# Optimization experiments

Measured on AMD Instinct MI355X. Metric: run time of the kernel, lower is better.

Reference implementation:

```python
import jax, jax.numpy as jnp
import numpy as np

N = 100000   # nodes
E = 1600000  # edges per view
F = 256      # feature_dim
G = 512      # num graphs in batch
H, C = 2, 32 # heads, channels per head (GATConv(F, 32, heads=2))
EPS = 1e-5


def setup_inputs() -> dict:
    key = jax.random.key(0)
    ks = jax.random.split(key, 32)
    def w(i, shape, fan_in):
        return jax.random.normal(ks[i], shape, jnp.float32) / np.sqrt(fan_in)
    inp = {
        "x": jax.random.normal(ks[0], (N, F), jnp.float32),
        "edge_index_ast": jax.random.randint(ks[1], (2, E), 0, N),
        "edge_index_cfg": jax.random.randint(ks[2], (2, E), 0, N),
        "edge_index_pdg": jax.random.randint(ks[3], (2, E), 0, N),
        "batch": jnp.sort(jax.random.randint(ks[4], (N,), 0, G)),
        "num_graphs": G,
        # BatchNorm1d(feature_dim) affine params (training-mode batch stats)
        "bn_w": jnp.ones((F,), jnp.float32),
        "bn_b": jnp.zeros((F,), jnp.float32),
    }
    i = 5
    for v in ("ast", "cfg", "pdg"):
        inp[f"{v}_W"] = w(i, (F, H * C), F); i += 1
        inp[f"{v}_att_src"] = w(i, (H, C), C); i += 1
        inp[f"{v}_att_dst"] = w(i, (H, C), C); i += 1
        inp[f"{v}_bias"] = jnp.zeros((H * C,), jnp.float32)
    inp["g1_w"] = w(i, (64, 32), 64); i += 1
    inp["g1_b"] = jnp.zeros((32,), jnp.float32)
    inp["g2_w"] = w(i, (32, 3), 32); i += 1
    inp["g2_b"] = jnp.zeros((3,), jnp.float32)
    inp["c1_w"] = w(i, (64, 128), 64); i += 1
    inp["c1_b"] = jnp.zeros((128,), jnp.float32)
    inp["c2_w"] = w(i, (128, 64), 128); i += 1
    inp["c2_b"] = jnp.zeros((64,), jnp.float32)
    inp["c3_w"] = w(i, (64, 1), 64); i += 1
    inp["c3_b"] = jnp.zeros((1,), jnp.float32)
    return inp


def _gat(x, edge_index, W, att_src, att_dst, bias):
    """PyG GATConv (shared lin, add_self_loops=True, concat heads)."""
    n = x.shape[0]
    loops = jnp.arange(n)
    src = jnp.concatenate([edge_index[0], loops])
    dst = jnp.concatenate([edge_index[1], loops])
    h = (x @ W).reshape(n, H, C)                       # [N,H,C]
    a_src = jnp.sum(h * att_src, axis=-1)              # [N,H]
    a_dst = jnp.sum(h * att_dst, axis=-1)              # [N,H]
    e = jax.nn.leaky_relu(a_src[src] + a_dst[dst], 0.2)  # [Etot,H]
    m = jax.ops.segment_max(e, dst, num_segments=n)
    p = jnp.exp(e - m[dst])
    denom = jax.ops.segment_sum(p, dst, num_segments=n)
    alpha = p / (denom[dst] + 1e-16)                   # [Etot,H]
    out = jax.ops.segment_sum(h[src] * alpha[:, :, None], dst, num_segments=n)
    return out.reshape(n, H * C) + bias


def reference(x, edge_index_ast, edge_index_cfg, edge_index_pdg, batch, num_graphs,
              bn_w, bn_b,
              ast_W, ast_att_src, ast_att_dst, ast_bias,
              cfg_W, cfg_att_src, cfg_att_dst, cfg_bias,
              pdg_W, pdg_att_src, pdg_att_dst, pdg_bias,
              g1_w, g1_b, g2_w, g2_b,
              c1_w, c1_b, c2_w, c2_b, c3_w, c3_b):
    # input BatchNorm1d (training-mode batch statistics, biased variance)
    mu = x.mean(0)
    var = x.var(0)
    xn = (x - mu) / jnp.sqrt(var + EPS) * bn_w + bn_b

    h_ast = jax.ops.segment_max(jax.nn.elu(_gat(xn, edge_index_ast, ast_W, ast_att_src, ast_att_dst, ast_bias)), batch, num_segments=num_graphs)
    h_cfg = jax.ops.segment_max(jax.nn.elu(_gat(xn, edge_index_cfg, cfg_W, cfg_att_src, cfg_att_dst, cfg_bias)), batch, num_segments=num_graphs)
    h_pdg = jax.ops.segment_max(jax.nn.elu(_gat(xn, edge_index_pdg, pdg_W, pdg_att_src, pdg_att_dst, pdg_bias)), batch, num_segments=num_graphs)

    avg_view = (h_ast + h_cfg + h_pdg) / 3.0
    wts = jax.nn.softmax(jax.nn.relu(avg_view @ g1_w + g1_b) @ g2_w + g2_b, axis=-1)
    fused = wts[:, 0:1] * h_ast + wts[:, 1:2] * h_cfg + wts[:, 2:3] * h_pdg

    # classifier (dropout = identity at inference)
    z = jax.nn.relu(fused @ c1_w + c1_b)
    z = jax.nn.relu(z @ c2_w + c2_b)
    logits = (z @ c3_w + c3_b).reshape(-1)             # [G]
    return logits
```

## Files before the change

kernel.cpp:

```cpp
#include <hip/hip_runtime.h>
#include <hip/hip_bf16.h>
#include <hip/hip_fp16.h>

#define N_NODES 100000
#define N_EDGES 1600000
#define ETOT    (N_EDGES + N_NODES)
#define NE3     (3 * ETOT)
#define N3      (3 * N_NODES)
#define NF      256
#define NG      512
#define NHC     64
#define NOUT3   192
#define BN_EPS  1e-5f

#define NBUCK   586
#define NB1     1024
#define EGRAIN  20
#define ECHUNK  (256 * EGRAIN)
#define SCAN_N  (NBUCK * NB1)
#define ATT2_NB (N_NODES * 16 / 256)

typedef _Float16 f16x8 __attribute__((ext_vector_type(8)));
typedef float    f32x4 __attribute__((ext_vector_type(4)));

__device__ __forceinline__ unsigned fenc(float f){
  unsigned b = __float_as_uint(f);
  return (b & 0x80000000u) ? ~b : (b | 0x80000000u);
}
__device__ __forceinline__ float fdec(unsigned u){
  unsigned b = (u & 0x80000000u) ? (u & 0x7FFFFFFFu) : ~u;
  return __uint_as_float(b);
}
__device__ __forceinline__ float lrelu(float x){ return x > 0.f ? x : 0.2f * x; }
__device__ __forceinline__ float eluf(float x){ return x > 0.f ? x : (__expf(x) - 1.f); }

__global__ void k_init_pooled(unsigned* pooled){
  int i = blockIdx.x * 256 + threadIdx.x;
  if (i < 3 * NG * NHC) pooled[i] = 0x007FFFFFu;
}

#define STATS_NB ((N_NODES + 127) / 128)
__global__ __launch_bounds__(256) void k_pre(const float* __restrict__ x,
                                             float* __restrict__ sums, float* __restrict__ sumsq,
                                             const int* __restrict__ eA, const int* __restrict__ eC,
                                             const int* __restrict__ eP,
                                             int* __restrict__ gcounts){
  int t = threadIdx.x;
  if (blockIdx.x < STATS_NB){
    int r0 = blockIdx.x * 128;
    int rmax = N_NODES - r0; if (rmax > 128) rmax = 128;
    float s = 0.f, q = 0.f;
    for (int r = 0; r < rmax; ++r){
      float v = x[(size_t)(r0 + r) * NF + t];
      s += v; q += v * v;
    }
    atomicAdd(&sums[t], s);
    atomicAdd(&sumsq[t], q);
    return;
  }
  __shared__ int hist[NBUCK];
  int bi = blockIdx.x - STATS_NB;
  for (int b = t; b < NBUCK; b += 256) hist[b] = 0;
  __syncthreads();
  int base = bi * ECHUNK + t;
#pragma unroll
  for (int k = 0; k < EGRAIN; ++k){
    int i = base + k * 256;
    if (i < NE3){
      int v = i / ETOT; int j = i - v * ETOT;
      const int* ei = (v == 0) ? eA : (v == 1) ? eC : eP;
      int d = (j < N_EDGES) ? ei[N_EDGES + j] : (j - N_EDGES);
      int vd = v * N_NODES + d;
      atomicAdd(&hist[vd >> 9], 1);
    }
  }
  __syncthreads();
  for (int b = t; b < NBUCK; b += 256) gcounts[b * NB1 + bi] = hist[b];
}

__global__ __launch_bounds__(256) void k_prep2(const float* __restrict__ sums, const float* __restrict__ sumsq,
                                               const float* __restrict__ bn_w, const float* __restrict__ bn_b,
                                               const float* __restrict__ WA, const float* __restrict__ WC,
                                               const float* __restrict__ WP,
                                               __half* __restrict__ WpT, float* __restrict__ bp){
  __shared__ float red[256];
  int o = blockIdx.x;
  int v = o >> 6, oc = o & 63;
  const float* W = (v == 0) ? WA : (v == 1) ? WC : WP;
  int f = threadIdx.x;
  float mu  = sums[f]  * (1.f / N_NODES);
  float var = sumsq[f] * (1.f / N_NODES) - mu * mu;
  float sc  = bn_w[f] * rsqrtf(var + BN_EPS);
  float sh_ = bn_b[f] - mu * sc;
  float w = W[f * 64 + oc];
  WpT[(size_t)o * NF + f] = __float2half(w * sc);
  red[f] = sh_ * w;
  __syncthreads();
  for (int off = 128; off > 0; off >>= 1){
    if (f < off) red[f] += red[f + off];
    __syncthreads();
  }
  if (f == 0) bp[o] = red[0];
}

__global__ __launch_bounds__(256) void k_avec(const float* __restrict__ sums, const float* __restrict__ sumsq,
                                              const float* __restrict__ bn_w, const float* __restrict__ bn_b,
                                              const float* __restrict__ WA, const float* __restrict__ asA, const float* __restrict__ adA,
                                              const float* __restrict__ WC, const float* __restrict__ asC, const float* __restrict__ adC,
                                              const float* __restrict__ WP, const float* __restrict__ asP, const float* __restrict__ adP,
                                              float* __restrict__ wvec, float* __restrict__ cbias){
  __shared__ float red[256];
  int f = threadIdx.x;
  float mu  = sums[f]  * (1.f / N_NODES);
  float var = sumsq[f] * (1.f / N_NODES) - mu * mu;
  float sc  = bn_w[f] * rsqrtf(var + BN_EPS);
  float sh_ = bn_b[f] - mu * sc;
  for (int v = 0; v < 3; ++v){
    const float* W  = (v == 0) ? WA : (v == 1) ? WC : WP;
    const float* As = (v == 0) ? asA : (v == 1) ? asC : asP;
    const float* Ad = (v == 0) ? adA : (v == 1) ? adC : adP;
    for (int h = 0; h < 2; ++h){
      float sa = 0.f, da = 0.f;
      for (int c = 0; c < 32; ++c){
        float w = W[f * 64 + h * 32 + c];
        sa += w * As[h * 32 + c];
        da += w * Ad[h * 32 + c];
      }
      int q = v * 2 + h;
      wvec[q * NF + f]       = sc * sa;
      wvec[(6 + q) * NF + f] = sc * da;
      red[f] = sh_ * sa; __syncthreads();
      for (int off = 128; off > 0; off >>= 1){ if (f < off) red[f] += red[f + off]; __syncthreads(); }
      if (f == 0) cbias[q] = red[0];
      __syncthreads();
      red[f] = sh_ * da; __syncthreads();
      for (int off = 128; off > 0; off >>= 1){ if (f < off) red[f] += red[f + off]; __syncthreads(); }
      if (f == 0) cbias[6 + q] = red[0];
      __syncthreads();
    }
  }
}

__global__ __launch_bounds__(256) void k_att2(const float* __restrict__ x,
                                              const float* __restrict__ wvec, const float* __restrict__ cbias,
                                              float* __restrict__ a_src, float* __restrict__ a_dst,
                                              unsigned* __restrict__ gpart){
  __shared__ float wv[12][256];
  __shared__ float cb[12];
  __shared__ unsigned samax[6];
  int t = threadIdx.x;
#pragma unroll
  for (int q = 0; q < 12; ++q) wv[q][t] = wvec[q * NF + t];
  if (t < 12) cb[t] = cbias[t];
  if (t < 6) samax[t] = 0u;
  __syncthreads();
  int grp = t >> 4, lid = t & 15;
  int n = blockIdx.x * 16 + grp;
  float4 xr[4];
#pragma unroll
  for (int k = 0; k < 4; ++k)
    xr[k] = *(const float4*)(x + (size_t)n * NF + k * 64 + lid * 4);
  float res[12];
#pragma unroll
  for (int q = 0; q < 12; ++q){
    float acc = 0.f;
#pragma unroll
    for (int k = 0; k < 4; ++k){
      float4 wq = *(const float4*)&wv[q][k * 64 + lid * 4];
      acc += xr[k].x * wq.x + xr[k].y * wq.y + xr[k].z * wq.z + xr[k].w * wq.w;
    }
    acc += __shfl_xor(acc, 1, 16);
    acc += __shfl_xor(acc, 2, 16);
    acc += __shfl_xor(acc, 4, 16);
    acc += __shfl_xor(acc, 8, 16);
    res[q] = acc + cb[q];
  }
  if (lid == 0){
#pragma unroll
    for (int v = 0; v < 3; ++v){
      int g = v * N_NODES + n;
      *(float2*)(a_src + (size_t)g * 2) = make_float2(res[v*2+0], res[v*2+1]);
      *(float2*)(a_dst + (size_t)g * 2) = make_float2(res[6+v*2+0], res[6+v*2+1]);
      atomicMax(&samax[v*2+0], fenc(res[v*2+0]));
      atomicMax(&samax[v*2+1], fenc(res[v*2+1]));
    }
  }
  __syncthreads();
  if (t < 6) gpart[blockIdx.x * 6 + t] = samax[t];
}

__global__ __launch_bounds__(256) void k_amax(const unsigned* __restrict__ gpart, unsigned* __restrict__ amax){
  __shared__ unsigned sm[6];
  int t = threadIdx.x;
  if (t < 6) sm[t] = 0u;
  __syncthreads();
  unsigned m[6] = {0u, 0u, 0u, 0u, 0u, 0u};
  for (int bi = t; bi < ATT2_NB; bi += 256){
    const unsigned* p = gpart + (size_t)bi * 6;
#pragma unroll
    for (int k = 0; k < 6; ++k) m[k] = max(m[k], p[k]);
  }
#pragma unroll
  for (int k = 0; k < 6; ++k) atomicMax(&sm[k], m[k]);
  __syncthreads();
  if (t < 6) amax[t] = sm[t];
}

__global__ __launch_bounds__(256) void k_scan1(const int* __restrict__ cnt, int* __restrict__ out,
                                               int* __restrict__ bsum, int n){
  __shared__ int sh[256];
  int t = threadIdx.x; int base = blockIdx.x * 2048 + t * 8;
  int v[8]; int s = 0;
#pragma unroll
  for (int i = 0; i < 8; ++i){ v[i] = (base + i < n) ? cnt[base + i] : 0; s += v[i]; }
  sh[t] = s; __syncthreads();
  for (int off = 1; off < 256; off <<= 1){
    int xv = (t >= off) ? sh[t - off] : 0;
    __syncthreads();
    sh[t] += xv;
    __syncthreads();
  }
  int p = sh[t] - s;
  if (t == 255) bsum[blockIdx.x] = sh[255];
#pragma unroll
  for (int i = 0; i < 8; ++i){ if (base + i < n) out[base + i] = p; p += v[i]; }
}

__global__ __launch_bounds__(512) void k_scan2(int* __restrict__ bsum, int* __restrict__ total_out, int nb){
  __shared__ int sh[512];
  int t = threadIdx.x;
  int o = (t < nb) ? bsum[t] : 0;
  sh[t] = o; __syncthreads();
  for (int off = 1; off < 512; off <<= 1){
    int xv = (t >= off) ? sh[t - off] : 0;
    __syncthreads();
    sh[t] += xv;
    __syncthreads();
  }
  if (t < nb) bsum[t] = sh[t] - o;
  if (t == nb - 1) total_out[0] = sh[t];
}

__global__ __launch_bounds__(256) void k_scan3(int* __restrict__ out, const int* __restrict__ bsum, int n){
  int add = bsum[blockIdx.x];
  int base = blockIdx.x * 2048 + threadIdx.x * 8;
#pragma unroll
  for (int i = 0; i < 8; ++i) if (base + i < n) out[base + i] += add;
}

#define GBM 64
#define GEMM_NB ((N_NODES + GBM - 1) / GBM)
__global__ __launch_bounds__(256) void k_fused(const float* __restrict__ x,
                                               const __half* __restrict__ WpT, const float* __restrict__ bp,
                                               __half* __restrict__ h16,
                                               const int* __restrict__ eA, const int* __restrict__ eC,
                                               const int* __restrict__ eP,
                                               const int* __restrict__ gscan, int* __restrict__ packed){
  union U { _Float16 xs[64 * 256]; int pos[NBUCK]; };
  __shared__ U sm;
  int t = threadIdx.x;
  if (blockIdx.x >= GEMM_NB){
    int bi = blockIdx.x - GEMM_NB;
    for (int b = t; b < NBUCK; b += 256) sm.pos[b] = gscan[b * NB1 + bi];
    __syncthreads();
    int base = bi * ECHUNK + t;
#pragma unroll
    for (int k = 0; k < EGRAIN; ++k){
      int i = base + k * 256;
      if (i < NE3){
        int v = i / ETOT; int j = i - v * ETOT;
        const int* ei = (v == 0) ? eA : (v == 1) ? eC : eP;
        int s, d;
        if (j < N_EDGES){ s = ei[j]; d = ei[N_EDGES + j]; } else { s = j - N_EDGES; d = s; }
        int vd = v * N_NODES + d;
        int p = atomicAdd(&sm.pos[vd >> 9], 1);
        packed[p] = s | ((vd & 511) << 17);
      }
    }
    return;
  }
  int m0 = blockIdx.x * GBM;
#pragma unroll
  for (int k = 0; k < 8; ++k){
    int G = t + k * 256;
    int row = G >> 5, g = G & 31;
    int grow = m0 + row; if (grow >= N_NODES) grow = N_NODES - 1;
    const float4* src = (const float4*)(x + (size_t)grow * NF + ((g ^ (row & 7)) << 3));
    float4 lo = src[0], hi = src[1];
    f16x8 h;
    h[0]=(_Float16)lo.x; h[1]=(_Float16)lo.y; h[2]=(_Float16)lo.z; h[3]=(_Float16)lo.w;
    h[4]=(_Float16)hi.x; h[5]=(_Float16)hi.y; h[6]=(_Float16)hi.z; h[7]=(_Float16)hi.w;
    *(f16x8*)&sm.xs[(size_t)G << 3] = h;
  }
  __syncthreads();
  int lane = t & 63, w = t >> 6;
  int lr = lane & 15, lk = lane >> 4;
  int colb = w * 48;
  f32x4 acc[4][3];
#pragma unroll
  for (int mt = 0; mt < 4; ++mt)
#pragma unroll
    for (int ct = 0; ct < 3; ++ct) acc[mt][ct] = (f32x4){0.f, 0.f, 0.f, 0.f};
  float bpv[3];
#pragma unroll
  for (int ct = 0; ct < 3; ++ct) bpv[ct] = bp[colb + ct * 16 + lr];
#pragma unroll
  for (int kk = 0; kk < 8; ++kk){
    int khalf = kk * 32 + lk * 8;
    f16x8 av[4];
#pragma unroll
    for (int mt = 0; mt < 4; ++mt){
      int row = mt * 16 + lr;
      av[mt] = *(const f16x8*)&sm.xs[row * 256 + (khalf ^ ((row & 7) << 3))];
    }
    f16x8 bv[3];
#pragma unroll
    for (int ct = 0; ct < 3; ++ct){
      int col = colb + ct * 16 + lr;
      bv[ct] = *(const f16x8*)(const void*)(WpT + (size_t)col * NF + khalf);
    }
#pragma unroll
    for (int mt = 0; mt < 4; ++mt)
#pragma unroll
      for (int ct = 0; ct < 3; ++ct)
        acc[mt][ct] = __builtin_amdgcn_mfma_f32_16x16x32_f16(av[mt], bv[ct], acc[mt][ct], 0, 0, 0);
  }
#pragma unroll
  for (int mt = 0; mt < 4; ++mt){
#pragma unroll
    for (int r = 0; r < 4; ++r){
      int row = m0 + mt * 16 + lk * 4 + r;
      if (row < N_NODES){
#pragma unroll
        for (int ct = 0; ct < 3; ++ct)
          h16[(size_t)row * NOUT3 + colb + ct * 16 + lr] = __float2half(acc[mt][ct][r] + bpv[ct]);
      }
    }
  }
}

__global__ __launch_bounds__(512) void k_build(const int* __restrict__ gscan, const int* __restrict__ packed,
                                               int* __restrict__ entries, int* __restrict__ offsets){
  __shared__ int hist2[512];
  __shared__ int sh[512];
  int b = blockIdx.x, t = threadIdx.x;
  int base = gscan[b * NB1];
  int end  = (b == NBUCK - 1) ? NE3 : gscan[(b + 1) * NB1];
  hist2[t] = 0;
  __syncthreads();
  for (int i = base + t; i < end; i += 512)
    atomicAdd(&hist2[(packed[i] >> 17) & 511], 1);
  __syncthreads();
  int cnt = hist2[t];
  sh[t] = cnt; __syncthreads();
  for (int off = 1; off < 512; off <<= 1){
    int xv = (t >= off) ? sh[t - off] : 0;
    __syncthreads();
    sh[t] += xv;
    __syncthreads();
  }
  int excl = sh[t] - cnt;
  hist2[t] = excl;
  int vd0 = (b << 9) + t;
  if (vd0 < N3) offsets[vd0] = base + excl;
  if (b == NBUCK - 1 && t == 0) offsets[N3] = NE3;
  __syncthreads();
  for (int i = base + t; i < end; i += 512){
    int pk = packed[i];
    int low = (pk >> 17) & 511;
    int pos = atomicAdd(&hist2[low], 1);
    entries[base + pos] = pk & 0x1FFFF;
  }
}

__global__ __launch_bounds__(256) void k_gather(const int* __restrict__ entries, const int* __restrict__ offsets,
                                                const float* __restrict__ a_src, const float* __restrict__ a_dst,
                                                const unsigned* __restrict__ amax,
                                                const __half* __restrict__ h16,
                                                const float* __restrict__ bA, const float* __restrict__ bC,
                                                const float* __restrict__ bP,
                                                const int* __restrict__ batch, unsigned* __restrict__ pooled){
  __shared__ unsigned red[64];
  __shared__ int kmin, kmax;
  int t = threadIdx.x;
  if (t == 0){ kmin = 0x7FFFFFFF; kmax = -1; }
  if (t < 64) red[t] = 0u;
  __syncthreads();
  int grp = t >> 4;
  int lid = t & 15;
  int g = blockIdx.x * 16 + grp;
  int v = g / N_NODES; int n = g - v * N_NODES;
  int vN = v * N_NODES;
  float ad0 = a_dst[g*2+0], ad1 = a_dst[g*2+1];
  float m0 = lrelu(fdec(amax[v*2+0]) + ad0);
  float m1 = lrelu(fdec(amax[v*2+1]) + ad1);
  int beg = offsets[g], end = offsets[g+1];
  int len = end - beg;
  float ax = 0.f, ay = 0.f, az = 0.f, aw = 0.f;
  float den0 = 0.f, den1 = 0.f;
  const __half* hbase = h16 + v * 64 + lid * 4;
  for (int c0 = 0; c0 < len; c0 += 16){
    int nc = len - c0; if (nc > 16) nc = 16;
    int s_ = 0; unsigned pu_ = 0u;
    if (lid < nc){
      s_ = entries[beg + c0 + lid];
      float2 ap = *(const float2*)(a_src + (size_t)(vN + s_) * 2);
      float p0 = __expf(lrelu(ap.x + ad0) - m0);
      float p1 = __expf(lrelu(ap.y + ad1) - m1);
      pu_ = (unsigned)__half_as_ushort(__float2half(p0))
          | ((unsigned)__half_as_ushort(__float2half(p1)) << 16);
    }
    den0 += __half2float(__ushort_as_half((unsigned short)(pu_ & 0xFFFFu)));
    den1 += __half2float(__ushort_as_half((unsigned short)(pu_ >> 16)));
    for (int k = 0; k < nc; k += 8){
      uint2 r[8]; float pa[8];
#pragma unroll
      for (int j = 0; j < 8; ++j){
        int kk = k + j;
        int sk = __shfl(s_, kk, 16);
        unsigned pk_ = (unsigned)__shfl((int)pu_, kk, 16);
        r[j] = *(const uint2*)(hbase + (size_t)sk * NOUT3);
        unsigned sel = (lid < 8) ? (pk_ & 0xFFFFu) : (pk_ >> 16);
        pa[j] = __half2float(__ushort_as_half((unsigned short)sel));
      }
#pragma unroll
      for (int j = 0; j < 8; ++j){
        float2 fa2 = __half22float2(*(__half2*)&r[j].x);
        float2 fb2 = __half22float2(*(__half2*)&r[j].y);
        ax = fmaf(pa[j], fa2.x, ax); ay = fmaf(pa[j], fa2.y, ay);
        az = fmaf(pa[j], fb2.x, az); aw = fmaf(pa[j], fb2.y, aw);
      }
    }
  }
#pragma unroll
  for (int msk = 1; msk < 16; msk <<= 1){
    den0 += __shfl_xor(den0, msk);
    den1 += __shfl_xor(den1, msk);
  }
  float den = ((lid < 8) ? den0 : den1) + 1e-16f;
  const float* bias = (v == 0) ? bA : (v == 1) ? bC : bP;
  float4 b4 = *(const float4*)(bias + lid * 4);
  unsigned e0u = fenc(eluf(ax / den + b4.x));
  unsigned e1u = fenc(eluf(ay / den + b4.y));
  unsigned e2u = fenc(eluf(az / den + b4.z));
  unsigned e3u = fenc(eluf(aw / den + b4.w));
  int key = v * NG + batch[n];
  if (lid == 0){ atomicMin(&kmin, key); atomicMax(&kmax, key); }
  atomicMax(&red[lid*4+0], e0u); atomicMax(&red[lid*4+1], e1u);
  atomicMax(&red[lid*4+2], e2u); atomicMax(&red[lid*4+3], e3u);
  __syncthreads();
  if (kmin == kmax){
    if (t < 64) atomicMax(&pooled[(size_t)kmin * 64 + t], red[t]);
  } else {
    unsigned* pp = pooled + (size_t)key * 64 + lid * 4;
    atomicMax(pp+0, e0u); atomicMax(pp+1, e1u); atomicMax(pp+2, e2u); atomicMax(pp+3, e3u);
  }
}

__global__ __launch_bounds__(64) void k_head(const unsigned* __restrict__ pooled,
                                             const float* __restrict__ g1w, const float* __restrict__ g1b,
                                             const float* __restrict__ g2w, const float* __restrict__ g2b,
                                             const float* __restrict__ c1w, const float* __restrict__ c1b,
                                             const float* __restrict__ c2w, const float* __restrict__ c2b,
                                             const float* __restrict__ c3w, const float* __restrict__ c3b,
                                             float* __restrict__ out){
  __shared__ float s1[64];
  __shared__ float s2[128];
  __shared__ float sw[3];
  int g = blockIdx.x, l = threadIdx.x;
  float ha = fdec(pooled[(size_t)g * 64 + l]);
  float hc = fdec(pooled[(size_t)(NG + g) * 64 + l]);
  float hp = fdec(pooled[(size_t)(2 * NG + g) * 64 + l]);
  s1[l] = (ha + hc + hp) * (1.f / 3.f);
  __syncthreads();
  float r1 = 0.f;
  if (l < 32){
    r1 = g1b[l];
    for (int i = 0; i < 64; ++i) r1 += s1[i] * g1w[i * 32 + l];
    r1 = fmaxf(r1, 0.f);
  }
  __syncthreads();
  if (l < 32) s2[l] = r1;
  __syncthreads();
  if (l < 3){
    float tv = g2b[l];
    for (int i = 0; i < 32; ++i) tv += s2[i] * g2w[i * 3 + l];
    sw[l] = tv;
  }
  __syncthreads();
  float t0 = sw[0], t1 = sw[1], t2 = sw[2];
  float mx = fmaxf(t0, fmaxf(t1, t2));
  float w0 = __expf(t0 - mx), w1 = __expf(t1 - mx), w2 = __expf(t2 - mx);
  float wsum = w0 + w1 + w2;
  float fused = (w0 * ha + w1 * hc + w2 * hp) / wsum;
  __syncthreads();
  s1[l] = fused;
  __syncthreads();
  float za = c1b[l], zb = c1b[64 + l];
  for (int i = 0; i < 64; ++i){
    float f = s1[i];
    za += f * c1w[i * 128 + l];
    zb += f * c1w[i * 128 + 64 + l];
  }
  za = fmaxf(za, 0.f); zb = fmaxf(zb, 0.f);
  s2[l] = za; s2[64 + l] = zb;
  __syncthreads();
  float z2 = c2b[l];
  for (int i = 0; i < 128; ++i) z2 += s2[i] * c2w[i * 64 + l];
  z2 = fmaxf(z2, 0.f);
  float prod = z2 * c3w[l];
  for (int off = 32; off > 0; off >>= 1) prod += __shfl_down(prod, off);
  if (l == 0) out[g] = prod + c3b[0];
}

extern "C" void kernel_launch(void* const* d_in, const int* in_sizes, int n_in,
                              void* d_out, int out_size, void* d_ws, size_t ws_size,
                              hipStream_t stream){
  const float* x    = (const float*)d_in[0];
  const int* eA     = (const int*)d_in[1];
  const int* eC     = (const int*)d_in[2];
  const int* eP     = (const int*)d_in[3];
  const int* batch  = (const int*)d_in[4];
  const float* bn_w = (const float*)d_in[6];
  const float* bn_b = (const float*)d_in[7];
  const float* WA   = (const float*)d_in[8];
  const float* asA  = (const float*)d_in[9];
  const float* adA  = (const float*)d_in[10];
  const float* bA   = (const float*)d_in[11];
  const float* WC   = (const float*)d_in[12];
  const float* asC  = (const float*)d_in[13];
  const float* adC  = (const float*)d_in[14];
  const float* bC   = (const float*)d_in[15];
  const float* WP   = (const float*)d_in[16];
  const float* asP  = (const float*)d_in[17];
  const float* adP  = (const float*)d_in[18];
  const float* bP   = (const float*)d_in[19];
  const float* g1w  = (const float*)d_in[20];
  const float* g1b  = (const float*)d_in[21];
  const float* g2w  = (const float*)d_in[22];
  const float* g2b  = (const float*)d_in[23];
  const float* c1w  = (const float*)d_in[24];
  const float* c1b  = (const float*)d_in[25];
  const float* c2w  = (const float*)d_in[26];
  const float* c2b  = (const float*)d_in[27];
  const float* c3w  = (const float*)d_in[28];
  const float* c3b  = (const float*)d_in[29];
  float* out = (float*)d_out;

  char* wptr = (char*)d_ws;
  auto alloc = [&](size_t bytes) -> void* {
    void* p = (void*)wptr;
    wptr += (bytes + 255) & ~(size_t)255;
    return p;
  };
  float*    sums    = (float*)   alloc((size_t)NF * 4);
  float*    sumsq   = (float*)   alloc((size_t)NF * 4);
  size_t zbytes = (size_t)(wptr - (char*)sums);
  int*      gcounts = (int*)     alloc((size_t)SCAN_N * 4);
  int*      gscan   = (int*)     alloc((size_t)SCAN_N * 4);
  int*      offsets = (int*)     alloc(((size_t)N3 + 1) * 4);
  __half*   WpT     = (__half*)  alloc((size_t)NOUT3 * NF * 2);
  float*    bp      = (float*)   alloc((size_t)NOUT3 * 4);
  float*    wvec    = (float*)   alloc((size_t)12 * NF * 4);
  float*    cbias   = (float*)   alloc((size_t)64 * 4);
  __half*   h16     = (__half*)  alloc((size_t)N_NODES * NOUT3 * 2);
  float*    a_src   = (float*)   alloc((size_t)N3 * 2 * 4);
  float*    a_dst   = (float*)   alloc((size_t)N3 * 2 * 4);
  int*      packed  = (int*)     alloc((size_t)NE3 * 4);
  int*      entries = (int*)     alloc((size_t)NE3 * 4);
  unsigned* pooled  = (unsigned*)alloc((size_t)3 * NG * NHC * 4);
  unsigned* gpart   = (unsigned*)alloc((size_t)ATT2_NB * 6 * 4);
  unsigned* amax    = (unsigned*)alloc((size_t)64 * 4);
  int*      bsum    = (int*)     alloc((size_t)512 * 4);
  int*      scrtot  = (int*)     alloc((size_t)64 * 4);

  hipMemsetAsync(sums, 0, zbytes, stream);
  k_init_pooled<<<(3 * NG * NHC + 255) / 256, 256, 0, stream>>>(pooled);
  k_pre<<<STATS_NB + NB1, 256, 0, stream>>>(x, sums, sumsq, eA, eC, eP, gcounts);
  k_prep2<<<NOUT3, 256, 0, stream>>>(sums, sumsq, bn_w, bn_b, WA, WC, WP, WpT, bp);
  k_avec<<<1, 256, 0, stream>>>(sums, sumsq, bn_w, bn_b, WA, asA, adA, WC, asC, adC, WP, asP, adP, wvec, cbias);
  int nb_sc = (SCAN_N + 2047) / 2048;
  k_scan1<<<nb_sc, 256, 0, stream>>>(gcounts, gscan, bsum, SCAN_N);
  k_scan2<<<1, 512, 0, stream>>>(bsum, scrtot, nb_sc);
  k_scan3<<<nb_sc, 256, 0, stream>>>(gscan, bsum, SCAN_N);
  k_att2<<<ATT2_NB, 256, 0, stream>>>(x, wvec, cbias, a_src, a_dst, gpart);
  k_amax<<<1, 256, 0, stream>>>(gpart, amax);
  k_fused<<<GEMM_NB + NB1, 256, 0, stream>>>(x, WpT, bp, h16, eA, eC, eP, gscan, packed);
  k_build<<<NBUCK, 512, 0, stream>>>(gscan, packed, entries, offsets);
  k_gather<<<N3 / 16, 256, 0, stream>>>(entries, offsets, a_src, a_dst, amax, h16, bA, bC, bP, batch, pooled);
  k_head<<<NG, 64, 0, stream>>>(pooled, g1w, g1b, g2w, g2b, c1w, c1b, c2w, c2b, c3w, c3b, out);
}
```

Measured before the change: 389.0 us.

## Fuse attention-logit and max kernels into GEMM/build launches; deterministic BN stats

Replaces the atomic BatchNorm stat accumulation with per-block partials and a separate reduction kernel, which drops the memset. It merges k_prep2 and k_avec into one launch. It folds the attention-logit computation into extra blocks of k_fused and the global max into block 0 of k_build, so fewer kernels launch and the att work overlaps the GEMM and scatter. The gather loop now keeps edge weights in fp32 and precomputes byte offsets, replacing the packed half weights. This adds one launch for the stats reduction, and block 0 of k_build carries extra serial work.

```diff
diff --git a/kernel.cpp b/kernel.cpp
--- a/kernel.cpp
+++ b/kernel.cpp
@@ -41,7 +41,7 @@
 
 #define STATS_NB ((N_NODES + 127) / 128)
 __global__ __launch_bounds__(256) void k_pre(const float* __restrict__ x,
-                                             float* __restrict__ sums, float* __restrict__ sumsq,
+                                             float* __restrict__ spartS, float* __restrict__ spartQ,
                                              const int* __restrict__ eA, const int* __restrict__ eC,
                                              const int* __restrict__ eP,
                                              int* __restrict__ gcounts){
@@ -54,8 +54,8 @@
       float v = x[(size_t)(r0 + r) * NF + t];
       s += v; q += v * v;
     }
-    atomicAdd(&sums[t], s);
-    atomicAdd(&sumsq[t], q);
+    spartS[(size_t)t * STATS_NB + blockIdx.x] = s;
+    spartQ[(size_t)t * STATS_NB + blockIdx.x] = q;
     return;
   }
   __shared__ int hist[NBUCK];
@@ -78,43 +78,52 @@
   for (int b = t; b < NBUCK; b += 256) gcounts[b * NB1 + bi] = hist[b];
 }
 
+__global__ __launch_bounds__(256) void k_stats2(const float* __restrict__ spartS, const float* __restrict__ spartQ,
+                                                float* __restrict__ sums, float* __restrict__ sumsq){
+  __shared__ float rs[256], rq[256];
+  int c = blockIdx.x, i = threadIdx.x;
+  float s = 0.f, q = 0.f;
+  for (int b = i; b < STATS_NB; b += 256){
+    s += spartS[(size_t)c * STATS_NB + b];
+    q += spartQ[(size_t)c * STATS_NB + b];
+  }
+  rs[i] = s; rq[i] = q;
+  __syncthreads();
+  for (int off = 128; off > 0; off >>= 1){
+    if (i < off){ rs[i] += rs[i + off]; rq[i] += rq[i + off]; }
+    __syncthreads();
+  }
+  if (i == 0){ sums[c] = rs[0]; sumsq[c] = rq[0]; }
+}
+
 __global__ __launch_bounds__(256) void k_prep2(const float* __restrict__ sums, const float* __restrict__ sumsq,
                                                const float* __restrict__ bn_w, const float* __restrict__ bn_b,
-                                               const float* __restrict__ WA, const float* __restrict__ WC,
-                                               const float* __restrict__ WP,
-                                               __half* __restrict__ WpT, float* __restrict__ bp){
-  __shared__ float red[256];
-  int o = blockIdx.x;
-  int v = o >> 6, oc = o & 63;
-  const float* W = (v == 0) ? WA : (v == 1) ? WC : WP;
-  int f = threadIdx.x;
-  float mu  = sums[f]  * (1.f / N_NODES);
-  float var = sumsq[f] * (1.f / N_NODES) - mu * mu;
-  float sc  = bn_w[f] * rsqrtf(var + BN_EPS);
-  float sh_ = bn_b[f] - mu * sc;
-  float w = W[f * 64 + oc];
-  WpT[(size_t)o * NF + f] = __float2half(w * sc);
-  red[f] = sh_ * w;
-  __syncthreads();
-  for (int off = 128; off > 0; off >>= 1){
-    if (f < off) red[f] += red[f + off];
-    __syncthreads();
-  }
-  if (f == 0) bp[o] = red[0];
-}
-
-__global__ __launch_bounds__(256) void k_avec(const float* __restrict__ sums, const float* __restrict__ sumsq,
-                                              const float* __restrict__ bn_w, const float* __restrict__ bn_b,
-                                              const float* __restrict__ WA, const float* __restrict__ asA, const float* __restrict__ adA,
-                                              const float* __restrict__ WC, const float* __restrict__ asC, const float* __restrict__ adC,
-                                              const float* __restrict__ WP, const float* __restrict__ asP, const float* __restrict__ adP,
-                                              float* __restrict__ wvec, float* __restrict__ cbias){
+                                               const float* __restrict__ WA, const float* __restrict__ asA, const float* __restrict__ adA,
+                                               const float* __restrict__ WC, const float* __restrict__ asC, const float* __restrict__ adC,
+                                               const float* __restrict__ WP, const float* __restrict__ asP, const float* __restrict__ adP,
+                                               __half* __restrict__ WpT, float* __restrict__ bp,
+                                               float* __restrict__ wvec, float* __restrict__ cbias){
   __shared__ float red[256];
   int f = threadIdx.x;
   float mu  = sums[f]  * (1.f / N_NODES);
   float var = sumsq[f] * (1.f / N_NODES) - mu * mu;
   float sc  = bn_w[f] * rsqrtf(var + BN_EPS);
   float sh_ = bn_b[f] - mu * sc;
+  int o = blockIdx.x;
+  if (o < NOUT3){
+    int v = o >> 6, oc = o & 63;
+    const float* W = (v == 0) ? WA : (v == 1) ? WC : WP;
+    float w = W[f * 64 + oc];
+    WpT[(size_t)o * NF + f] = __float2half(w * sc);
+    red[f] = sh_ * w;
+    __syncthreads();
+    for (int off = 128; off > 0; off >>= 1){
+      if (f < off) red[f] += red[f + off];
+      __syncthreads();
+    }
+    if (f == 0) bp[o] = red[0];
+    return;
+  }
   for (int v = 0; v < 3; ++v){
     const float* W  = (v == 0) ? WA : (v == 1) ? WC : WP;
     const float* As = (v == 0) ? asA : (v == 1) ? asC : asP;
@@ -141,71 +150,6 @@
   }
 }
 
-__global__ __launch_bounds__(256) void k_att2(const float* __restrict__ x,
-                                              const float* __restrict__ wvec, const float* __restrict__ cbias,
-                                              float* __restrict__ a_src, float* __restrict__ a_dst,
-                                              unsigned* __restrict__ gpart){
-  __shared__ float wv[12][256];
-  __shared__ float cb[12];
-  __shared__ unsigned samax[6];
-  int t = threadIdx.x;
-#pragma unroll
-  for (int q = 0; q < 12; ++q) wv[q][t] = wvec[q * NF + t];
-  if (t < 12) cb[t] = cbias[t];
-  if (t < 6) samax[t] = 0u;
-  __syncthreads();
-  int grp = t >> 4, lid = t & 15;
-  int n = blockIdx.x * 16 + grp;
-  float4 xr[4];
-#pragma unroll
-  for (int k = 0; k < 4; ++k)
-    xr[k] = *(const float4*)(x + (size_t)n * NF + k * 64 + lid * 4);
-  float res[12];
-#pragma unroll
-  for (int q = 0; q < 12; ++q){
-    float acc = 0.f;
-#pragma unroll
-    for (int k = 0; k < 4; ++k){
-      float4 wq = *(const float4*)&wv[q][k * 64 + lid * 4];
-      acc += xr[k].x * wq.x + xr[k].y * wq.y + xr[k].z * wq.z + xr[k].w * wq.w;
-    }
-    acc += __shfl_xor(acc, 1, 16);
-    acc += __shfl_xor(acc, 2, 16);
-    acc += __shfl_xor(acc, 4, 16);
-    acc += __shfl_xor(acc, 8, 16);
-    res[q] = acc + cb[q];
-  }
-  if (lid == 0){
-#pragma unroll
-    for (int v = 0; v < 3; ++v){
-      int g = v * N_NODES + n;
-      *(float2*)(a_src + (size_t)g * 2) = make_float2(res[v*2+0], res[v*2+1]);
-      *(float2*)(a_dst + (size_t)g * 2) = make_float2(res[6+v*2+0], res[6+v*2+1]);
-      atomicMax(&samax[v*2+0], fenc(res[v*2+0]));
-      atomicMax(&samax[v*2+1], fenc(res[v*2+1]));
-    }
-  }
-  __syncthreads();
-  if (t < 6) gpart[blockIdx.x * 6 + t] = samax[t];
-}
-
-__global__ __launch_bounds__(256) void k_amax(const unsigned* __restrict__ gpart, unsigned* __restrict__ amax){
-  __shared__ unsigned sm[6];
-  int t = threadIdx.x;
-  if (t < 6) sm[t] = 0u;
-  __syncthreads();
-  unsigned m[6] = {0u, 0u, 0u, 0u, 0u, 0u};
-  for (int bi = t; bi < ATT2_NB; bi += 256){
-    const unsigned* p = gpart + (size_t)bi * 6;
-#pragma unroll
-    for (int k = 0; k < 6; ++k) m[k] = max(m[k], p[k]);
-  }
-#pragma unroll
-  for (int k = 0; k < 6; ++k) atomicMax(&sm[k], m[k]);
-  __syncthreads();
-  if (t < 6) amax[t] = sm[t];
-}
-
 __global__ __launch_bounds__(256) void k_scan1(const int* __restrict__ cnt, int* __restrict__ out,
                                                int* __restrict__ bsum, int n){
   __shared__ int sh[256];
@@ -255,10 +199,59 @@
                                                __half* __restrict__ h16,
                                                const int* __restrict__ eA, const int* __restrict__ eC,
                                                const int* __restrict__ eP,
-                                               const int* __restrict__ gscan, int* __restrict__ packed){
-  union U { _Float16 xs[64 * 256]; int pos[NBUCK]; };
+                                               const int* __restrict__ gscan, int* __restrict__ packed,
+                                               const float* __restrict__ wvec, const float* __restrict__ cbias,
+                                               float* __restrict__ a_src, float* __restrict__ a_dst,
+                                               unsigned* __restrict__ gpart){
+  union U {
+    _Float16 xs[64 * 256];
+    int pos[NBUCK];
+    struct { float wv[12][256]; float cb[12]; unsigned samax[6]; } att;
+  };
   __shared__ U sm;
   int t = threadIdx.x;
+  if (blockIdx.x >= GEMM_NB + NB1){
+    int abi = blockIdx.x - (GEMM_NB + NB1);
+#pragma unroll
+    for (int q = 0; q < 12; ++q) sm.att.wv[q][t] = wvec[q * NF + t];
+    if (t < 12) sm.att.cb[t] = cbias[t];
+    if (t < 6) sm.att.samax[t] = 0u;
+    __syncthreads();
+    int grp = t >> 4, lid = t & 15;
+    int n = abi * 16 + grp;
+    float4 xr[4];
+#pragma unroll
+    for (int k = 0; k < 4; ++k)
+      xr[k] = *(const float4*)(x + (size_t)n * NF + k * 64 + lid * 4);
+    float res[12];
+#pragma unroll
+    for (int q = 0; q < 12; ++q){
+      float acc = 0.f;
+#pragma unroll
+      for (int k = 0; k < 4; ++k){
+        float4 wq = *(const float4*)&sm.att.wv[q][k * 64 + lid * 4];
+        acc += xr[k].x * wq.x + xr[k].y * wq.y + xr[k].z * wq.z + xr[k].w * wq.w;
+      }
+      acc += __shfl_xor(acc, 1, 16);
+      acc += __shfl_xor(acc, 2, 16);
+      acc += __shfl_xor(acc, 4, 16);
+      acc += __shfl_xor(acc, 8, 16);
+      res[q] = acc + sm.att.cb[q];
+    }
+    if (lid == 0){
+#pragma unroll
+      for (int v = 0; v < 3; ++v){
+        int g = v * N_NODES + n;
+        *(float2*)(a_src + (size_t)g * 2) = make_float2(res[v*2+0], res[v*2+1]);
+        *(float2*)(a_dst + (size_t)g * 2) = make_float2(res[6+v*2+0], res[6+v*2+1]);
+        atomicMax(&sm.att.samax[v*2+0], fenc(res[v*2+0]));
+        atomicMax(&sm.att.samax[v*2+1], fenc(res[v*2+1]));
+      }
+    }
+    __syncthreads();
+    if (t < 6) gpart[abi * 6 + t] = sm.att.samax[t];
+    return;
+  }
   if (blockIdx.x >= GEMM_NB){
     int bi = blockIdx.x - GEMM_NB;
     for (int b = t; b < NBUCK; b += 256) sm.pos[b] = gscan[b * NB1 + bi];
@@ -340,10 +333,26 @@
 }
 
 __global__ __launch_bounds__(512) void k_build(const int* __restrict__ gscan, const int* __restrict__ packed,
-                                               int* __restrict__ entries, int* __restrict__ offsets){
+                                               int* __restrict__ entries, int* __restrict__ offsets,
+                                               const unsigned* __restrict__ gpart, unsigned* __restrict__ amax){
   __shared__ int hist2[512];
   __shared__ int sh[512];
+  __shared__ unsigned smx[6];
   int b = blockIdx.x, t = threadIdx.x;
+  if (b == 0){
+    if (t < 6) smx[t] = 0u;
+    __syncthreads();
+    unsigned m[6] = {0u, 0u, 0u, 0u, 0u, 0u};
+    for (int bi = t; bi < ATT2_NB; bi += 512){
+      const unsigned* p = gpart + (size_t)bi * 6;
+#pragma unroll
+      for (int k = 0; k < 6; ++k) m[k] = max(m[k], p[k]);
+    }
+#pragma unroll
+    for (int k = 0; k < 6; ++k) atomicMax(&smx[k], m[k]);
+    __syncthreads();
+    if (t < 6) amax[t] = smx[t];
+  }
   int base = gscan[b * NB1];
   int end  = (b == NBUCK - 1) ? NE3 : gscan[(b + 1) * NB1];
   hist2[t] = 0;
@@ -398,30 +407,30 @@
   int len = end - beg;
   float ax = 0.f, ay = 0.f, az = 0.f, aw = 0.f;
   float den0 = 0.f, den1 = 0.f;
-  const __half* hbase = h16 + v * 64 + lid * 4;
+  const char* hb = (const char*)h16;
+  unsigned lconst = (unsigned)((v << 7) + (lid << 3));
   for (int c0 = 0; c0 < len; c0 += 16){
     int nc = len - c0; if (nc > 16) nc = 16;
-    int s_ = 0; unsigned pu_ = 0u;
+    unsigned off_ = 0u;
+    float p0f = 0.f, p1f = 0.f;
     if (lid < nc){
-      s_ = entries[beg + c0 + lid];
+      int s_ = entries[beg + c0 + lid];
       float2 ap = *(const float2*)(a_src + (size_t)(vN + s_) * 2);
-      float p0 = __expf(lrelu(ap.x + ad0) - m0);
-      float p1 = __expf(lrelu(ap.y + ad1) - m1);
-      pu_ = (unsigned)__half_as_ushort(__float2half(p0))
-          | ((unsigned)__half_as_ushort(__float2half(p1)) << 16);
-    }
-    den0 += __half2float(__ushort_as_half((unsigned short)(pu_ & 0xFFFFu)));
-    den1 += __half2float(__ushort_as_half((unsigned short)(pu_ >> 16)));
+      p0f = __expf(lrelu(ap.x + ad0) - m0);
+      p1f = __expf(lrelu(ap.y + ad1) - m1);
+      off_ = (unsigned)s_ * (NOUT3 * 2);
+    }
+    den0 += p0f; den1 += p1f;
     for (int k = 0; k < nc; k += 8){
       uint2 r[8]; float pa[8];
 #pragma unroll
       for (int j = 0; j < 8; ++j){
         int kk = k + j;
-        int sk = __shfl(s_, kk, 16);
-        unsigned pk_ = (unsigned)__shfl((int)pu_, kk, 16);
-        r[j] = *(const uint2*)(hbase + (size_t)sk * NOUT3);
-        unsigned sel = (lid < 8) ? (pk_ & 0xFFFFu) : (pk_ >> 16);
-        pa[j] = __half2float(__ushort_as_half((unsigned short)sel));
+        unsigned ob = (unsigned)__shfl((int)off_, kk, 16) + lconst;
+        float pA = __shfl(p0f, kk, 16);
+        float pB = __shfl(p1f, kk, 16);
+        r[j] = *(const uint2*)(hb + ob);
+        pa[j] = (lid < 8) ? pA : pB;
       }
 #pragma unroll
       for (int j = 0; j < 8; ++j){
@@ -555,7 +564,8 @@
   };
   float*    sums    = (float*)   alloc((size_t)NF * 4);
   float*    sumsq   = (float*)   alloc((size_t)NF * 4);
-  size_t zbytes = (size_t)(wptr - (char*)sums);
+  float*    spartS  = (float*)   alloc((size_t)NF * STATS_NB * 4);
+  float*    spartQ  = (float*)   alloc((size_t)NF * STATS_NB * 4);
   int*      gcounts = (int*)     alloc((size_t)SCAN_N * 4);
   int*      gscan   = (int*)     alloc((size_t)SCAN_N * 4);
   int*      offsets = (int*)     alloc(((size_t)N3 + 1) * 4);
@@ -574,19 +584,20 @@
   int*      bsum    = (int*)     alloc((size_t)512 * 4);
   int*      scrtot  = (int*)     alloc((size_t)64 * 4);
 
-  hipMemsetAsync(sums, 0, zbytes, stream);
   k_init_pooled<<<(3 * NG * NHC + 255) / 256, 256, 0, stream>>>(pooled);
-  k_pre<<<STATS_NB + NB1, 256, 0, stream>>>(x, sums, sumsq, eA, eC, eP, gcounts);
-  k_prep2<<<NOUT3, 256, 0, stream>>>(sums, sumsq, bn_w, bn_b, WA, WC, WP, WpT, bp);
-  k_avec<<<1, 256, 0, stream>>>(sums, sumsq, bn_w, bn_b, WA, asA, adA, WC, asC, adC, WP, asP, adP, wvec, cbias);
+  k_pre<<<STATS_NB + NB1, 256, 0, stream>>>(x, spartS, spartQ, eA, eC, eP, gcounts);
+  k_stats2<<<NF, 256, 0, stream>>>(spartS, spartQ, sums, sumsq);
+  k_prep2<<<NOUT3 + 1, 256, 0, stream>>>(sums, sumsq, bn_w, bn_b,
+                                         WA, asA, adA, WC, asC, adC, WP, asP, adP,
+                                         WpT, bp, wvec, cbias);
   int nb_sc = (SCAN_N + 2047) / 2048;
   k_scan1<<<nb_sc, 256, 0, stream>>>(gcounts, gscan, bsum, SCAN_N);
   k_scan2<<<1, 512, 0, stream>>>(bsum, scrtot, nb_sc);
   k_scan3<<<nb_sc, 256, 0, stream>>>(gscan, bsum, SCAN_N);
-  k_att2<<<ATT2_NB, 256, 0, stream>>>(x, wvec, cbias, a_src, a_dst, gpart);
-  k_amax<<<1, 256, 0, stream>>>(gpart, amax);
-  k_fused<<<GEMM_NB + NB1, 256, 0, stream>>>(x, WpT, bp, h16, eA, eC, eP, gscan, packed);
-  k_build<<<NBUCK, 512, 0, stream>>>(gscan, packed, entries, offsets);
+  k_fused<<<GEMM_NB + NB1 + ATT2_NB, 256, 0, stream>>>(x, WpT, bp, h16, eA, eC, eP,
+                                                       gscan, packed, wvec, cbias,
+                                                       a_src, a_dst, gpart);
+  k_build<<<NBUCK, 512, 0, stream>>>(gscan, packed, entries, offsets, gpart, amax);
   k_gather<<<N3 / 16, 256, 0, stream>>>(entries, offsets, a_src, a_dst, amax, h16, bA, bC, bP, batch, pooled);
   k_head<<<NG, 64, 0, stream>>>(pooled, g1w, g1b, g2w, g2b, c1w, c1b, c2w, c2b, c3w, c3b, out);
 }
```

New measurement: 380.1 us. 1.02x faster.
